# Kernel tuning notes

Measured on AMD Instinct MI355X. Metric: run time of the kernel, lower is better.

## Reference

```python
import jax, jax.numpy as jnp
import numpy as np

V, E, H, L, B, T = 8192, 64, 256, 2, 4, 512


def setup_inputs() -> dict:
    key = jax.random.key(0)
    ks = jax.random.split(key, 20)
    s = 0.02
    emb = (jax.random.normal(ks[0], (V, E)) * s).at[0].set(0.0)  # padding_idx=0
    x = jax.random.randint(ks[1], (B, T), 0, V)
    return {
        "x": x,
        "emb": emb,
        "W_ih0": jax.random.normal(ks[2], (H, E)) * s,
        "W_hh0": jax.random.normal(ks[3], (H, H)) * s,
        "b_ih0": jnp.zeros((H,), jnp.float32),
        "b_hh0": jnp.zeros((H,), jnp.float32),
        "W_ih1": jax.random.normal(ks[4], (H, H)) * s,
        "W_hh1": jax.random.normal(ks[5], (H, H)) * s,
        "b_ih1": jnp.zeros((H,), jnp.float32),
        "b_hh1": jnp.zeros((H,), jnp.float32),
        "Wq": jax.random.normal(ks[6], (H, H)) * s,
        "Wk": jax.random.normal(ks[7], (H, H)) * s,
        "v": jax.random.normal(ks[8], (H,)) * s,
        "gamma": jnp.ones((2 * H,), jnp.float32),
        "beta": jnp.zeros((2 * H,), jnp.float32),
        "Wfc": jax.random.normal(ks[9], (V, 2 * H)) * s,
        "bfc": jnp.zeros((V,), jnp.float32),
    }


def _rnn_layer(xs, W_ih, W_hh, b_ih, b_hh):
    # xs: (B, T, D) -> ys: (B, T, H), hT: (B, H). Vanilla tanh RNN.
    Bn = xs.shape[0]
    Hn = W_hh.shape[0]
    h0 = jnp.zeros((Bn, Hn), xs.dtype)

    def step(h, xt):
        h_new = jnp.tanh(xt @ W_ih.T + b_ih + h @ W_hh.T + b_hh)
        return h_new, h_new

    hT, ys = jax.lax.scan(step, h0, jnp.swapaxes(xs, 0, 1))
    return jnp.swapaxes(ys, 0, 1), hT


def reference(x, emb, W_ih0, W_hh0, b_ih0, b_hh0, W_ih1, W_hh1, b_ih1, b_hh1,
              Wq, Wk, v, gamma, beta, Wfc, bfc):
    # Dropout layers are identity (eval mode).
    e = emb[x]                                   # (B, T, E)
    y0, h0 = _rnn_layer(e, W_ih0, W_hh0, b_ih0, b_hh0)
    y1, h1 = _rnn_layer(y0, W_ih1, W_hh1, b_ih1, b_hh1)  # (B, T, H)

    # Bahdanau additive attention with causal mask
    q = y1 @ Wq.T                                # (B, T, H)
    k = y1 @ Wk.T                                # (B, T, H)
    # (B, Tq, Tk, H) broadcast add -> tanh -> contract with v
    scores = jnp.einsum('bijh,h->bij', jnp.tanh(q[:, :, None, :] + k[:, None, :, :]), v)
    Tn = scores.shape[1]
    causal = jnp.tril(jnp.ones((Tn, Tn), bool))
    scores = jnp.where(causal[None], scores, jnp.float32(-1e9))
    alpha = jax.nn.softmax(scores, axis=-1)      # (B, Tq, Tk)
    ctx = jnp.einsum('bij,bjh->bih', alpha, y1)  # bmm(alpha, K) with K = rnn_out

    cat = jnp.concatenate([y1, ctx], axis=-1)    # (B, T, 2H)
    mu = cat.mean(-1, keepdims=True)
    var = ((cat - mu) ** 2).mean(-1, keepdims=True)
    normed = (cat - mu) / jnp.sqrt(var + 1e-5) * gamma + beta

    logits = normed @ Wfc.T + bfc                # (B, T, V)
    h = jnp.stack([h0, h1], axis=0)              # (L, B, H)
    return logits, h
```

## Files before the change

### kernel.cpp

```cpp
#include <hip/hip_runtime.h>
#include <hip/hip_bf16.h>

typedef __bf16 bf16x8 __attribute__((ext_vector_type(8)));
typedef float  f32x4  __attribute__((ext_vector_type(4)));
typedef unsigned short u16;

#define T_N 512
#define H_N 256
#define B_N 4
#define V_N 8192
#define E_N 64

__device__ __forceinline__ float tanh_fast(float x) {
    float e = __expf(2.0f * x);
    return 1.0f - __fdividef(2.0f, e + 1.0f);
}

__device__ __forceinline__ u16 f2bf(float f) {
    __hip_bfloat16 h = __float2bfloat16(f);
    return __builtin_bit_cast(u16, h);
}

__device__ __forceinline__ bf16x8 as_bf16x8(uint4 u) {
    return __builtin_bit_cast(bf16x8, u);
}

__device__ __forceinline__ uint4 pack_bf8(f32x4 lo, f32x4 hi) {
    union { u16 s[8]; uint4 u; } r;
    #pragma unroll
    for (int e = 0; e < 4; ++e) { r.s[e] = f2bf(lo[e]); r.s[e+4] = f2bf(hi[e]); }
    return r.u;
}

__device__ __forceinline__ f32x4 mfma16(bf16x8 a, bf16x8 b, f32x4 c) {
    return __builtin_amdgcn_mfma_f32_16x16x32_bf16(a, b, c, 0, 0, 0);
}

__global__ void cvt_bf16_kernel(const float* __restrict__ src, u16* __restrict__ dst, int n4) {
    int i = blockIdx.x * 256 + threadIdx.x;
    if (i < n4) {
        f32x4 v = ((const f32x4*)src)[i];
        union { u16 s[4]; unsigned long long u; } r;
        #pragma unroll
        for (int e = 0; e < 4; ++e) r.s[e] = f2bf(v[e]);
        ((unsigned long long*)dst)[i] = r.u;
    }
}

__global__ __launch_bounds__(256)
void embed_xw0_kernel(const int* __restrict__ x, const float* __restrict__ emb,
                      const float* __restrict__ Wih, const float* __restrict__ bih,
                      const float* __restrict__ bhh, float* __restrict__ xw0) {
    const int t = blockIdx.x, tid = threadIdx.x;
    __shared__ float sE[4][64];
    {
        const int b = tid >> 6, k = tid & 63;
        sE[b][k] = emb[(size_t)x[b * T_N + t] * E_N + k];
    }
    __syncthreads();
    const int j = tid;
    const float* wr = Wih + j * E_N;
    float a0 = 0, a1 = 0, a2 = 0, a3 = 0;
    #pragma unroll 8
    for (int k = 0; k < E_N; ++k) {
        float wv = wr[k];
        a0 += sE[0][k] * wv; a1 += sE[1][k] * wv;
        a2 += sE[2][k] * wv; a3 += sE[3][k] * wv;
    }
    const float bs = bih[j] + bhh[j];
    f32x4 o = { a0 + bs, a1 + bs, a2 + bs, a3 + bs };
    *(f32x4*)(xw0 + ((size_t)t * H_N + j) * 4) = o;
}

template<int STORE_F32>
__global__ __launch_bounds__(256, 1)
void rnn_rec_kernel(const float* __restrict__ Whh, const float* __restrict__ xw,
                    u16* __restrict__ ybf, float* __restrict__ yf32,
                    float* __restrict__ hT) {
    __shared__ __align__(16) u16   hbuf[2][16][H_N];
    __shared__ __align__(16) float tmp[4][64][4];

    const int tid = threadIdx.x;
    const int w = tid >> 6, l = tid & 63;
    const int m = l & 15, g = l >> 4;
    const int jmy = (w << 6) + l;

    for (int idx = tid; idx < 2 * 16 * H_N; idx += 256) (&hbuf[0][0][0])[idx] = 0;

    bf16x8 wfrag[4][8];
    #pragma unroll
    for (int nt = 0; nt < 4; ++nt) {
        const int j = (w << 6) + (nt << 4) + m;
        #pragma unroll
        for (int kk = 0; kk < 8; ++kk) {
            const float* p = Whh + (size_t)j * H_N + (kk << 5) + (g << 3);
            f32x4 lo = *(const f32x4*)p;
            f32x4 hi = *(const f32x4*)(p + 4);
            wfrag[nt][kk] = as_bf16x8(pack_bf8(lo, hi));
        }
    }

    const f32x4* xwv = (const f32x4*)xw;
    f32x4 xw_cur = xwv[jmy];
    __syncthreads();

    int cur = 0;
    for (int t = 0; t < T_N; ++t) {
        const int tn = (t + 1 < T_N) ? (t + 1) : t;
        f32x4 xw_nxt = xwv[(size_t)tn * H_N + jmy];

        bf16x8 af[8];
        const char* hb = (const char*)&hbuf[cur][0][0];
        #pragma unroll
        for (int kk = 0; kk < 8; ++kk) {
            int byte = (m << 9) + (kk << 6) + (g << 4);
            byte ^= (m & 7) << 4;
            af[kk] = as_bf16x8(*(const uint4*)(hb + byte));
        }

        f32x4 c[4];
        #pragma unroll
        for (int nt = 0; nt < 4; ++nt) c[nt] = (f32x4){0.f, 0.f, 0.f, 0.f};
        #pragma unroll
        for (int kk = 0; kk < 8; ++kk)
            #pragma unroll
            for (int nt = 0; nt < 4; ++nt)
                c[nt] = mfma16(af[kk], wfrag[nt][kk], c[nt]);

        if (g == 0) {
            #pragma unroll
            for (int nt = 0; nt < 4; ++nt)
                *(f32x4*)&tmp[w][(nt << 4) + m][0] = c[nt];
        }
        f32x4 hv = *(const f32x4*)&tmp[w][l][0];
        hv += xw_cur;

        char* hbn = (char*)&hbuf[cur ^ 1][0][0];
        #pragma unroll
        for (int b = 0; b < 4; ++b) {
            float hn = tanh_fast(hv[b]);
            u16 bits = f2bf(hn);
            int byte = (b << 9) + (jmy << 1);
            byte ^= (b & 7) << 4;
            *(u16*)(hbn + byte) = bits;
            ybf[((size_t)b * T_N + t) * H_N + jmy] = bits;
            if (STORE_F32) yf32[((size_t)b * T_N + t) * H_N + jmy] = hn;
            if (t == T_N - 1) hT[b * H_N + jmy] = hn;
        }
        xw_cur = xw_nxt;
        cur ^= 1;
        __syncthreads();
    }
}

template<int MODE>
__global__ __launch_bounds__(256, 2)
void gemm_bf16(const u16* __restrict__ A, const u16* __restrict__ Bw,
               float* __restrict__ out, const float* __restrict__ bias,
               const float* __restrict__ bias2, int M, int N, int K) {
    __shared__ __align__(16) u16 As[64][40];
    __shared__ __align__(16) u16 Bs[64][40];
    const int tid = threadIdx.x;
    const int nb = N >> 6;
    const int bm = blockIdx.x / nb, bn = blockIdx.x % nb;
    const int l = tid & 63, w = tid >> 6;
    const int wm = w & 1, wn = w >> 1;
    const int m = l & 15, g = l >> 4;
    const int srow = tid >> 2, sseg = tid & 3;

    f32x4 c[2][2];
    #pragma unroll
    for (int i = 0; i < 2; ++i)
        #pragma unroll
        for (int j = 0; j < 2; ++j) c[i][j] = (f32x4){0.f, 0.f, 0.f, 0.f};

    const u16* ap = A  + (size_t)(bm * 64 + srow) * K + sseg * 8;
    const u16* bp = Bw + (size_t)(bn * 64 + srow) * K + sseg * 8;

    for (int k0 = 0; k0 < K; k0 += 32) {
        uint4 av = *(const uint4*)(ap + k0);
        uint4 bv = *(const uint4*)(bp + k0);
        __syncthreads();
        *(uint4*)&As[srow][sseg << 3] = av;
        *(uint4*)&Bs[srow][sseg << 3] = bv;
        __syncthreads();
        bf16x8 af[2], bfr[2];
        #pragma unroll
        for (int i = 0; i < 2; ++i) {
            af[i]  = as_bf16x8(*(const uint4*)&As[(wm << 5) + (i << 4) + m][g << 3]);
            bfr[i] = as_bf16x8(*(const uint4*)&Bs[(wn << 5) + (i << 4) + m][g << 3]);
        }
        #pragma unroll
        for (int i = 0; i < 2; ++i)
            #pragma unroll
            for (int j = 0; j < 2; ++j)
                c[i][j] = mfma16(af[i], bfr[j], c[i][j]);
    }

    #pragma unroll
    for (int i = 0; i < 2; ++i)
        #pragma unroll
        for (int j = 0; j < 2; ++j) {
            const int col = (bn << 6) + (wn << 5) + (j << 4) + m;
            float bs = 0.f;
            if (bias)  bs += bias[col];
            if (bias2) bs += bias2[col];
            #pragma unroll
            for (int r = 0; r < 4; ++r) {
                const int row = (bm << 6) + (wm << 5) + (i << 4) + (g << 2) + r;
                const float val = c[i][j][r] + bs;
                if (MODE == 0) {
                    out[(size_t)row * N + col] = val;
                } else if (MODE == 1) {
                    const int b = row >> 9, t = row & 511;
                    out[((size_t)t * N + col) * 4 + b] = val;
                } else {
                    const int b = row >> 9, t = row & 511;
                    out[(size_t)b * N * T_N + (size_t)col * T_N + t] = val;
                }
            }
        }
}

__global__ __launch_bounds__(256)
void attn_kernel(const float* __restrict__ q, const float* __restrict__ kT,
                 const float* __restrict__ y1f, const float* __restrict__ vvec,
                 float* __restrict__ ctx) {
    const int blk = blockIdx.x;
    const int b = blk >> 9, i = blk & 511;
    const int tid = threadIdx.x;
    __shared__ float sQ[H_N], sV[H_N], sS[T_N];
    __shared__ float red[4];
    sQ[tid] = q[((size_t)b * T_N + i) * H_N + tid];
    sV[tid] = vvec[tid];
    __syncthreads();

    float s0 = -1e30f, s1 = -1e30f;
    if (tid <= i) {
        const float* kp = kT + (size_t)b * H_N * T_N + tid;
        float acc = 0.f;
        for (int h = 0; h < H_N; ++h) acc += sV[h] * tanh_fast(sQ[h] + kp[(size_t)h * T_N]);
        s0 = acc;
    }
    if (tid + 256 <= i) {
        const float* kp = kT + (size_t)b * H_N * T_N + tid + 256;
        float acc = 0.f;
        for (int h = 0; h < H_N; ++h) acc += sV[h] * tanh_fast(sQ[h] + kp[(size_t)h * T_N]);
        s1 = acc;
    }
    float mv = fmaxf(s0, s1);
    #pragma unroll
    for (int o = 32; o; o >>= 1) mv = fmaxf(mv, __shfl_xor(mv, o, 64));
    if ((tid & 63) == 0) red[tid >> 6] = mv;
    __syncthreads();
    mv = fmaxf(fmaxf(red[0], red[1]), fmaxf(red[2], red[3]));
    __syncthreads();
    float e0 = (tid <= i)       ? __expf(s0 - mv) : 0.f;
    float e1 = (tid + 256 <= i) ? __expf(s1 - mv) : 0.f;
    float sm = e0 + e1;
    #pragma unroll
    for (int o = 32; o; o >>= 1) sm += __shfl_xor(sm, o, 64);
    if ((tid & 63) == 0) red[tid >> 6] = sm;
    __syncthreads();
    sm = red[0] + red[1] + red[2] + red[3];
    const float rs = 1.0f / sm;
    sS[tid] = e0 * rs;
    sS[tid + 256] = e1 * rs;
    __syncthreads();
    float acc = 0.f;
    const float* yp = y1f + (size_t)b * T_N * H_N + tid;
    for (int j2 = 0; j2 <= i; ++j2) acc += sS[j2] * yp[(size_t)j2 * H_N];
    ctx[((size_t)b * T_N + i) * H_N + tid] = acc;
}

__global__ __launch_bounds__(256)
void ln_kernel(const float* __restrict__ y1f, const float* __restrict__ ctx,
               const float* __restrict__ gamma, const float* __restrict__ beta,
               u16* __restrict__ outbf) {
    const int row = blockIdx.x, tid = threadIdx.x;
    __shared__ float red[4];
    const float x1 = y1f[(size_t)row * H_N + tid];
    const float x2 = ctx[(size_t)row * H_N + tid];
    float s = x1 + x2;
    #pragma unroll
    for (int o = 32; o; o >>= 1) s += __shfl_xor(s, o, 64);
    if ((tid & 63) == 0) red[tid >> 6] = s;
    __syncthreads();
    const float mu = (red[0] + red[1] + red[2] + red[3]) * (1.f / 512.f);
    __syncthreads();
    const float d1 = x1 - mu, d2 = x2 - mu;
    float qv = d1 * d1 + d2 * d2;
    #pragma unroll
    for (int o = 32; o; o >>= 1) qv += __shfl_xor(qv, o, 64);
    if ((tid & 63) == 0) red[tid >> 6] = qv;
    __syncthreads();
    const float var = (red[0] + red[1] + red[2] + red[3]) * (1.f / 512.f);
    const float inv = rsqrtf(var + 1e-5f);
    outbf[(size_t)row * 512 + tid]       = f2bf(d1 * inv * gamma[tid] + beta[tid]);
    outbf[(size_t)row * 512 + tid + 256] = f2bf(d2 * inv * gamma[tid + 256] + beta[tid + 256]);
}

extern "C" void kernel_launch(void* const* d_in, const int* in_sizes, int n_in,
                              void* d_out, int out_size, void* d_ws, size_t ws_size,
                              hipStream_t stream) {
    const int*   x     = (const int*)  d_in[0];
    const float* emb   = (const float*)d_in[1];
    const float* Wih0  = (const float*)d_in[2];
    const float* Whh0  = (const float*)d_in[3];
    const float* bih0  = (const float*)d_in[4];
    const float* bhh0  = (const float*)d_in[5];
    const float* Wih1  = (const float*)d_in[6];
    const float* Whh1  = (const float*)d_in[7];
    const float* bih1  = (const float*)d_in[8];
    const float* bhh1  = (const float*)d_in[9];
    const float* Wq    = (const float*)d_in[10];
    const float* Wk    = (const float*)d_in[11];
    const float* vvec  = (const float*)d_in[12];
    const float* gamma = (const float*)d_in[13];
    const float* beta  = (const float*)d_in[14];
    const float* Wfc   = (const float*)d_in[15];
    const float* bfc   = (const float*)d_in[16];

    float* outp = (float*)d_out;
    char* ws = (char*)d_ws;
    float* xw0   = (float*)(ws + 0);
    float* xw1   = (float*)(ws + 2097152);
    u16*   y0bf  = (u16*)  (ws + 4194304);
    u16*   y1bf  = (u16*)  (ws + 5242880);
    float* y1f   = (float*)(ws + 6291456);
    float* qf    = (float*)(ws + 8388608);
    float* kT    = (float*)(ws + 10485760);
    float* ctx   = (float*)(ws + 12582912);
    u16*   nrm   = (u16*)  (ws + 14680064);
    u16*   Wih1b = (u16*)  (ws + 16777216);
    u16*   Wqb   = (u16*)  (ws + 16908288);
    u16*   Wkb   = (u16*)  (ws + 17039360);
    u16*   Wfcb  = (u16*)  (ws + 17170432);

    float* hout = outp + (size_t)B_N * T_N * V_N;

    cvt_bf16_kernel<<<64,   256, 0, stream>>>(Wih1, Wih1b, 65536 / 4);
    cvt_bf16_kernel<<<64,   256, 0, stream>>>(Wq,   Wqb,   65536 / 4);
    cvt_bf16_kernel<<<64,   256, 0, stream>>>(Wk,   Wkb,   65536 / 4);
    cvt_bf16_kernel<<<4096, 256, 0, stream>>>(Wfc,  Wfcb,  4194304 / 4);

    embed_xw0_kernel<<<512, 256, 0, stream>>>(x, emb, Wih0, bih0, bhh0, xw0);
    rnn_rec_kernel<0><<<1, 256, 0, stream>>>(Whh0, xw0, y0bf, nullptr, hout);
    gemm_bf16<1><<<32 * 4, 256, 0, stream>>>(y0bf, Wih1b, xw1, bih1, bhh1, 2048, 256, 256);
    rnn_rec_kernel<1><<<1, 256, 0, stream>>>(Whh1, xw1, y1bf, y1f, hout + 1024);
    gemm_bf16<0><<<32 * 4, 256, 0, stream>>>(y1bf, Wqb, qf, nullptr, nullptr, 2048, 256, 256);
    gemm_bf16<2><<<32 * 4, 256, 0, stream>>>(y1bf, Wkb, kT, nullptr, nullptr, 2048, 256, 256);
    attn_kernel<<<2048, 256, 0, stream>>>(qf, kT, y1f, vvec, ctx);
    ln_kernel<<<2048, 256, 0, stream>>>(y1f, ctx, gamma, beta, nrm);
    gemm_bf16<0><<<32 * 128, 256, 0, stream>>>(nrm, Wfcb, outp, bfc, nullptr, 2048, 8192, 512);
}
```

Measured before the change: 963.1 us.

## Streamline RNN recurrence step and add larger-tile FC GEMM kernel

The recurrence kernel now stores only the 4 real batch rows of h in a padded LDS buffer. Lanes read their own batch row directly, and the MFMA chain is split into two independent accumulators that are summed in registers, which removes the tmp round trip through LDS. The full __syncthreads is replaced by an explicit lgkmcnt wait plus s_barrier to shorten the serial per-step latency. The final vocab projection moves to a new 128x128-tile GEMM with swizzled LDS for more operand reuse per block, at the cost of more registers and fewer blocks.

```diff
diff --git a/kernel.cpp b/kernel.cpp
--- a/kernel.cpp
+++ b/kernel.cpp
@@ -77,15 +77,15 @@
 void rnn_rec_kernel(const float* __restrict__ Whh, const float* __restrict__ xw,
                     u16* __restrict__ ybf, float* __restrict__ yf32,
                     float* __restrict__ hT) {
-    __shared__ __align__(16) u16   hbuf[2][16][H_N];
-    __shared__ __align__(16) float tmp[4][64][4];
+    __shared__ __align__(16) u16 hbuf[2][4][288];
 
     const int tid = threadIdx.x;
     const int w = tid >> 6, l = tid & 63;
     const int m = l & 15, g = l >> 4;
+    const int b4 = m & 3;
     const int jmy = (w << 6) + l;
 
-    for (int idx = tid; idx < 2 * 16 * H_N; idx += 256) (&hbuf[0][0][0])[idx] = 0;
+    for (int idx = tid; idx < 2 * 4 * 288; idx += 256) (&hbuf[0][0][0])[idx] = (u16)0;
 
     bf16x8 wfrag[4][8];
     #pragma unroll
@@ -110,46 +110,45 @@
         f32x4 xw_nxt = xwv[(size_t)tn * H_N + jmy];
 
         bf16x8 af[8];
-        const char* hb = (const char*)&hbuf[cur][0][0];
-        #pragma unroll
-        for (int kk = 0; kk < 8; ++kk) {
-            int byte = (m << 9) + (kk << 6) + (g << 4);
-            byte ^= (m & 7) << 4;
-            af[kk] = as_bf16x8(*(const uint4*)(hb + byte));
-        }
-
-        f32x4 c[4];
-        #pragma unroll
-        for (int nt = 0; nt < 4; ++nt) c[nt] = (f32x4){0.f, 0.f, 0.f, 0.f};
         #pragma unroll
         for (int kk = 0; kk < 8; ++kk)
+            af[kk] = as_bf16x8(*(const uint4*)&hbuf[cur][b4][(kk << 5) + (g << 3)]);
+
+        f32x4 ca[4], cb[4];
+        #pragma unroll
+        for (int nt = 0; nt < 4; ++nt) {
+            ca[nt] = (f32x4){0.f, 0.f, 0.f, 0.f};
+            cb[nt] = (f32x4){0.f, 0.f, 0.f, 0.f};
+        }
+        #pragma unroll
+        for (int kk = 0; kk < 4; ++kk)
             #pragma unroll
-            for (int nt = 0; nt < 4; ++nt)
-                c[nt] = mfma16(af[kk], wfrag[nt][kk], c[nt]);
-
-        if (g == 0) {
-            #pragma unroll
-            for (int nt = 0; nt < 4; ++nt)
-                *(f32x4*)&tmp[w][(nt << 4) + m][0] = c[nt];
-        }
-        f32x4 hv = *(const f32x4*)&tmp[w][l][0];
+            for (int nt = 0; nt < 4; ++nt) {
+                ca[nt] = mfma16(af[kk],     wfrag[nt][kk],     ca[nt]);
+                cb[nt] = mfma16(af[kk + 4], wfrag[nt][kk + 4], cb[nt]);
+            }
+
+        f32x4 hv = (g == 0) ? (ca[0] + cb[0])
+                 : (g == 1) ? (ca[1] + cb[1])
+                 : (g == 2) ? (ca[2] + cb[2])
+                 :            (ca[3] + cb[3]);
         hv += xw_cur;
 
-        char* hbn = (char*)&hbuf[cur ^ 1][0][0];
         #pragma unroll
         for (int b = 0; b < 4; ++b) {
             float hn = tanh_fast(hv[b]);
             u16 bits = f2bf(hn);
-            int byte = (b << 9) + (jmy << 1);
-            byte ^= (b & 7) << 4;
-            *(u16*)(hbn + byte) = bits;
+            hbuf[cur ^ 1][b][jmy] = bits;
             ybf[((size_t)b * T_N + t) * H_N + jmy] = bits;
             if (STORE_F32) yf32[((size_t)b * T_N + t) * H_N + jmy] = hn;
             if (t == T_N - 1) hT[b * H_N + jmy] = hn;
         }
         xw_cur = xw_nxt;
         cur ^= 1;
-        __syncthreads();
+
+        asm volatile("s_waitcnt lgkmcnt(0)" ::: "memory");
+        __builtin_amdgcn_s_barrier();
+        __builtin_amdgcn_sched_barrier(0);
     }
 }
 
@@ -218,6 +217,73 @@
                     const int b = row >> 9, t = row & 511;
                     out[(size_t)b * N * T_N + (size_t)col * T_N + t] = val;
                 }
+            }
+        }
+}
+
+__global__ __launch_bounds__(256, 2)
+void gemm_fc(const u16* __restrict__ A, const u16* __restrict__ Bw,
+             const float* __restrict__ bias, float* __restrict__ out) {
+    __shared__ __align__(16) u16 As[128 * 32];
+    __shared__ __align__(16) u16 Bs[128 * 32];
+    const int tid = threadIdx.x;
+    const int l = tid & 63, w = tid >> 6;
+    const int m = l & 15, g = l >> 4;
+    const int wm = w >> 1, wn = w & 1;
+    const int bm = blockIdx.x >> 6, bn = blockIdx.x & 63;
+    constexpr int K = 512;
+
+    f32x4 acc[4][4];
+    #pragma unroll
+    for (int i = 0; i < 4; ++i)
+        #pragma unroll
+        for (int j = 0; j < 4; ++j) acc[i][j] = (f32x4){0.f, 0.f, 0.f, 0.f};
+
+    const u16* aBase = A  + (size_t)(bm * 128) * K;
+    const u16* bBase = Bw + (size_t)(bn * 128) * K;
+    const int row0 = tid >> 2,          seg0 = tid & 3;
+    const int row1 = (tid + 256) >> 2,  seg1 = tid & 3;
+    const int wseg0 = seg0 ^ ((row0 >> 1) & 3);
+    const int wseg1 = seg1 ^ ((row1 >> 1) & 3);
+
+    for (int k0 = 0; k0 < K; k0 += 32) {
+        uint4 av0 = *(const uint4*)(aBase + (size_t)row0 * K + k0 + seg0 * 8);
+        uint4 av1 = *(const uint4*)(aBase + (size_t)row1 * K + k0 + seg1 * 8);
+        uint4 bv0 = *(const uint4*)(bBase + (size_t)row0 * K + k0 + seg0 * 8);
+        uint4 bv1 = *(const uint4*)(bBase + (size_t)row1 * K + k0 + seg1 * 8);
+        __syncthreads();
+        *(uint4*)((char*)As + row0 * 64 + wseg0 * 16) = av0;
+        *(uint4*)((char*)As + row1 * 64 + wseg1 * 16) = av1;
+        *(uint4*)((char*)Bs + row0 * 64 + wseg0 * 16) = bv0;
+        *(uint4*)((char*)Bs + row1 * 64 + wseg1 * 16) = bv1;
+        __syncthreads();
+        bf16x8 af[4], bfr[4];
+        #pragma unroll
+        for (int i = 0; i < 4; ++i) {
+            const int arow = wm * 64 + i * 16 + m;
+            const int aslot = g ^ ((arow >> 1) & 3);
+            af[i]  = as_bf16x8(*(const uint4*)((char*)As + arow * 64 + aslot * 16));
+            const int brow = wn * 64 + i * 16 + m;
+            const int bslot = g ^ ((brow >> 1) & 3);
+            bfr[i] = as_bf16x8(*(const uint4*)((char*)Bs + brow * 64 + bslot * 16));
+        }
+        #pragma unroll
+        for (int i = 0; i < 4; ++i)
+            #pragma unroll
+            for (int j = 0; j < 4; ++j)
+                acc[i][j] = mfma16(af[i], bfr[j], acc[i][j]);
+    }
+
+    #pragma unroll
+    for (int i = 0; i < 4; ++i)
+        #pragma unroll
+        for (int j = 0; j < 4; ++j) {
+            const int col = bn * 128 + wn * 64 + j * 16 + m;
+            const float bs = bias[col];
+            #pragma unroll
+            for (int r = 0; r < 4; ++r) {
+                const int row = bm * 128 + wm * 64 + i * 16 + (g << 2) + r;
+                out[(size_t)row * V_N + col] = acc[i][j][r] + bs;
             }
         }
 }
@@ -352,5 +418,5 @@
     gemm_bf16<2><<<32 * 4, 256, 0, stream>>>(y1bf, Wkb, kT, nullptr, nullptr, 2048, 256, 256);
     attn_kernel<<<2048, 256, 0, stream>>>(qf, kT, y1f, vvec, ctx);
     ln_kernel<<<2048, 256, 0, stream>>>(y1f, ctx, gamma, beta, nrm);
-    gemm_bf16<0><<<32 * 128, 256, 0, stream>>>(nrm, Wfcb, outp, bfc, nullptr, 2048, 8192, 512);
-}
+    gemm_fc<<<16 * 64, 256, 0, stream>>>(nrm, Wfcb, bfc, outp);
+}
```

Result: slower. 1.023 ms (+6.2%).
